# Kernel tuning notes

Measured on AMD Instinct MI355X. Metric: run time of the kernel, lower is better.

Reference implementation:

```python
import jax, jax.numpy as jnp
import numpy as np

DECAY = 0.9  # decay_const buffer (learn_decay=False)


def setup_inputs() -> dict:
    key = jax.random.key(0)
    ks = jax.random.split(key, 6)
    B, T, D = 64, 512, 768
    spk_hist = jax.random.normal(ks[0], (B, T, D), dtype=jnp.float32)
    act_hist = jax.random.normal(ks[1], (B, T, D), dtype=jnp.float32)
    spk_mask = jax.random.randint(ks[2], (B, T), 0, 2).astype(jnp.float32)
    act_mask = jax.random.randint(ks[3], (B, T), 0, 2).astype(jnp.float32)
    spk_mean = jax.random.normal(ks[4], (B, D), dtype=jnp.float32)
    act_mean = jax.random.normal(ks[5], (B, D), dtype=jnp.float32)
    mix_logits = jnp.zeros((2,), dtype=jnp.float32)
    return {"spk_hist": spk_hist, "spk_mask": spk_mask,
            "act_hist": act_hist, "act_mask": act_mask,
            "spk_mean": spk_mean, "act_mean": act_mean,
            "mix_logits": mix_logits}


def ema_pool(X, mask, decay):
    # X: [B,T,D], mask: [B,T] (1 valid, 0 pad) -> (h [B,D], has_any [B])
    B, T, D = X.shape
    one_minus = 1.0 - decay

    def step(carry, xm):
        h, has_any = carry          # [B,D], [B,1]
        xt, mt = xm                 # [B,D], [B]
        mt = mt[:, None]            # [B,1]
        h_new = decay * h + one_minus * xt
        h = mt * h_new + (1.0 - mt) * h
        has_any = jnp.minimum(has_any + mt, 1.0)
        return (h, has_any), None

    h0 = jnp.zeros((B, D), X.dtype)
    a0 = jnp.zeros((B, 1), X.dtype)
    (h, has_any), _ = jax.lax.scan(
        step, (h0, a0), (jnp.swapaxes(X, 0, 1), mask.T))
    return h, has_any[:, 0]


def reference(spk_hist, spk_mask, act_hist, act_mask, spk_mean, act_mean, mix_logits):
    c_spk, spk_nonempty = ema_pool(spk_hist, spk_mask, DECAY)
    c_act, act_nonempty = ema_pool(act_hist, act_mask, DECAY)
    c_spk = jnp.where((spk_nonempty == 0)[:, None], spk_mean, c_spk)
    c_act = jnp.where((act_nonempty == 0)[:, None], act_mean, c_act)
    w = jax.nn.softmax(mix_logits, axis=0)
    c = w[0] * c_spk + w[1] * c_act
    return (c, c_spk, c_act, w)
```

## Files before the change

kernel.cpp:

```cpp
#include <hip/hip_runtime.h>

#define B 64
#define T 512
#define D 768
#define NSEG 8
#define TSEG 64
#define LOG2_DECAY (-0.15200309344504995f)

#define WS_H  0
#define WS_NE (2 * B * D)
#define WS_W  (2 * B * D + 2 * B)

__global__ __launch_bounds__(512) void weights_kernel(
    const float* __restrict__ spk_mask, const float* __restrict__ act_mask,
    float* __restrict__ ws)
{
    const int b = blockIdx.x & (B - 1);
    const int s = blockIdx.x >> 6;
    const float* mask = s ? act_mask : spk_mask;

    const int t = threadIdx.x;
    const float m = mask[b * T + t];
    const bool on = m > 0.5f;

    const unsigned long long bal = __ballot(on);
    const int lane = t & 63;
    const int wave = t >> 6;

    __shared__ int wtot[8];
    if (lane == 0) wtot[wave] = __popcll(bal);
    __syncthreads();

    int Ct = __popcll(bal & (~0ull >> (63 - lane)));
    int S = 0;
    #pragma unroll
    for (int i = 0; i < 8; ++i) {
        int c = wtot[i];
        if (i < wave) Ct += c;
        S += c;
    }

    const float w = on ? 0.1f * exp2f((float)(S - Ct) * LOG2_DECAY) : 0.0f;
    ws[WS_W + (s * B + b) * T + t] = w;
    if (t == 0) ws[WS_NE + s * B + b] = (S > 0) ? 1.0f : 0.0f;
}

__global__ __launch_bounds__(192) void pool_kernel(
    const float* __restrict__ spk_hist, const float* __restrict__ act_hist,
    float* __restrict__ ws)
{
    const int blk = blockIdx.x;
    const int seg = blk & (NSEG - 1);
    const int b   = (blk >> 3) & (B - 1);
    const int s   = blk >> 9;

    __shared__ float wsm[TSEG];
    const int tid = threadIdx.x;
    if (tid < TSEG)
        wsm[tid] = ws[WS_W + (s * B + b) * T + seg * TSEG + tid];
    __syncthreads();

    const float* hist = s ? act_hist : spk_hist;
    const float4* X = (const float4*)(hist + (size_t)(b * T + seg * TSEG) * D) + tid;

    float4 acc = make_float4(0.f, 0.f, 0.f, 0.f);
    for (int tt = 0; tt < TSEG; ++tt) {
        const float w = wsm[tt];
        if (w != 0.0f) {
            const float4 x = X[tt * (D / 4)];
            acc.x = fmaf(w, x.x, acc.x);
            acc.y = fmaf(w, x.y, acc.y);
            acc.z = fmaf(w, x.z, acc.z);
            acc.w = fmaf(w, x.w, acc.w);
        }
    }

    float* hdst = ws + WS_H + (size_t)(s * B + b) * D + tid * 4;
    atomicAdd(hdst + 0, acc.x);
    atomicAdd(hdst + 1, acc.y);
    atomicAdd(hdst + 2, acc.z);
    atomicAdd(hdst + 3, acc.w);
}

__global__ __launch_bounds__(256) void epilogue_kernel(
    const float* __restrict__ spk_mean, const float* __restrict__ act_mean,
    const float* __restrict__ logits, const float* __restrict__ ws,
    float* __restrict__ out)
{
    const int idx = blockIdx.x * 256 + threadIdx.x;
    if (idx >= B * D) return;
    const int b = idx / D;

    const float l0 = logits[0], l1 = logits[1];
    const float mx = fmaxf(l0, l1);
    const float e0 = expf(l0 - mx), e1 = expf(l1 - mx);
    const float inv = 1.0f / (e0 + e1);
    const float w0 = e0 * inv, w1 = e1 * inv;

    const float cs = (ws[WS_NE + b]     > 0.0f) ? ws[WS_H + idx]          : spk_mean[idx];
    const float ca = (ws[WS_NE + B + b] > 0.0f) ? ws[WS_H + B * D + idx]  : act_mean[idx];

    out[idx]             = w0 * cs + w1 * ca;
    out[B * D + idx]     = cs;
    out[2 * B * D + idx] = ca;
    if (idx == 0) {
        out[3 * B * D]     = w0;
        out[3 * B * D + 1] = w1;
    }
}

extern "C" void kernel_launch(void* const* d_in, const int* in_sizes, int n_in,
                              void* d_out, int out_size, void* d_ws, size_t ws_size,
                              hipStream_t stream) {
    const float* spk_hist = (const float*)d_in[0];
    const float* spk_mask = (const float*)d_in[1];
    const float* act_hist = (const float*)d_in[2];
    const float* act_mask = (const float*)d_in[3];
    const float* spk_mean = (const float*)d_in[4];
    const float* act_mean = (const float*)d_in[5];
    const float* logits   = (const float*)d_in[6];
    float* ws  = (float*)d_ws;
    float* out = (float*)d_out;

    hipMemsetAsync(ws, 0, (size_t)(2 * B * D) * sizeof(float), stream);

    weights_kernel<<<2 * B, 512, 0, stream>>>(spk_mask, act_mask, ws);
    pool_kernel<<<2 * B * NSEG, 192, 0, stream>>>(spk_hist, act_hist, ws);
    epilogue_kernel<<<(B * D + 255) / 256, 256, 0, stream>>>(spk_mean, act_mean, logits, ws, out);
}
```

Baseline: 217.0 us.

## Fuse mask weight computation into pool kernel and replace atomics with partial sums

Drops the separate weights kernel and the memset. Each pool block recomputes the mask prefix counts and decay weights for its own segment, then compacts the valid timesteps so the load loop runs only over them, unrolled by four. Per-segment partial sums are written to the workspace without atomics and reduced in a vectorised epilogue. This removes two launches and the atomic traffic, at the cost of redundant mask scans in every block and an extra partial-sum buffer pass.

Result: faster. 207.9 us (-4.2%).

```diff
diff --git a/kernel.cpp b/kernel.cpp
--- a/kernel.cpp
+++ b/kernel.cpp
@@ -7,46 +7,12 @@
 #define TSEG 64
 #define LOG2_DECAY (-0.15200309344504995f)
 
-#define WS_H  0
-#define WS_NE (2 * B * D)
-#define WS_W  (2 * B * D + 2 * B)
-
-__global__ __launch_bounds__(512) void weights_kernel(
-    const float* __restrict__ spk_mask, const float* __restrict__ act_mask,
-    float* __restrict__ ws)
-{
-    const int b = blockIdx.x & (B - 1);
-    const int s = blockIdx.x >> 6;
-    const float* mask = s ? act_mask : spk_mask;
-
-    const int t = threadIdx.x;
-    const float m = mask[b * T + t];
-    const bool on = m > 0.5f;
-
-    const unsigned long long bal = __ballot(on);
-    const int lane = t & 63;
-    const int wave = t >> 6;
-
-    __shared__ int wtot[8];
-    if (lane == 0) wtot[wave] = __popcll(bal);
-    __syncthreads();
-
-    int Ct = __popcll(bal & (~0ull >> (63 - lane)));
-    int S = 0;
-    #pragma unroll
-    for (int i = 0; i < 8; ++i) {
-        int c = wtot[i];
-        if (i < wave) Ct += c;
-        S += c;
-    }
-
-    const float w = on ? 0.1f * exp2f((float)(S - Ct) * LOG2_DECAY) : 0.0f;
-    ws[WS_W + (s * B + b) * T + t] = w;
-    if (t == 0) ws[WS_NE + s * B + b] = (S > 0) ? 1.0f : 0.0f;
-}
+#define WS_P  0
+#define WS_NE (2 * B * NSEG * D)
 
 __global__ __launch_bounds__(192) void pool_kernel(
     const float* __restrict__ spk_hist, const float* __restrict__ act_hist,
+    const float* __restrict__ spk_mask, const float* __restrict__ act_mask,
     float* __restrict__ ws)
 {
     const int blk = blockIdx.x;
@@ -54,32 +20,93 @@
     const int b   = (blk >> 3) & (B - 1);
     const int s   = blk >> 9;
 
-    __shared__ float wsm[TSEG];
-    const int tid = threadIdx.x;
-    if (tid < TSEG)
-        wsm[tid] = ws[WS_W + (s * B + b) * T + seg * TSEG + tid];
+    const int tid  = threadIdx.x;
+    const int lane = tid & 63;
+    const int wave = tid >> 6;
+
+    __shared__ float    wsm[TSEG];
+    __shared__ float    cw[TSEG];
+    __shared__ int      ct[TSEG];
+    __shared__ unsigned wt[2];
+    __shared__ int      Mcnt;
+
+    const float* mask = s ? act_mask : spk_mask;
+    unsigned bits = 0, cnt = 0;
+    if (tid < 128) {
+        const float4 mv = ((const float4*)(mask + b * T))[tid];
+        bits = (mv.x > 0.5f ? 1u : 0u) | (mv.y > 0.5f ? 2u : 0u) |
+               (mv.z > 0.5f ? 4u : 0u) | (mv.w > 0.5f ? 8u : 0u);
+        cnt = __popc(bits);
+    }
+    unsigned v = cnt;
+    #pragma unroll
+    for (int off = 1; off < 64; off <<= 1) {
+        const unsigned u = __shfl_up(v, off);
+        if (lane >= off) v += u;
+    }
+    if (wave < 2 && lane == 63) wt[wave] = v;
+    __syncthreads();
+    const unsigned S = wt[0] + wt[1];
+
+    if (tid >= seg * 16 && tid < (seg + 1) * 16) {
+        unsigned run = (v - cnt) + (wave == 1 ? wt[0] : 0u);
+        const int lbase = (tid - seg * 16) * 4;
+        #pragma unroll
+        for (int j = 0; j < 4; ++j) {
+            float w = 0.0f;
+            if (bits & (1u << j)) {
+                run += 1;
+                w = 0.1f * exp2f((float)(S - run) * LOG2_DECAY);
+            }
+            wsm[lbase + j] = w;
+        }
+    }
+    __syncthreads();
+
+    if (tid < 64) {
+        const float wv = wsm[tid];
+        const unsigned long long bal = __ballot(wv != 0.0f);
+        if (wv != 0.0f) {
+            const int pos = __popcll(bal & ((1ull << tid) - 1ull));
+            cw[pos] = wv;
+            ct[pos] = tid;
+        }
+        if (tid == 0) Mcnt = __popcll(bal);
+    }
     __syncthreads();
 
     const float* hist = s ? act_hist : spk_hist;
-    const float4* X = (const float4*)(hist + (size_t)(b * T + seg * TSEG) * D) + tid;
+    const float* Xb = hist + (size_t)(b * T + seg * TSEG) * D + tid * 4;
 
     float4 acc = make_float4(0.f, 0.f, 0.f, 0.f);
-    for (int tt = 0; tt < TSEG; ++tt) {
-        const float w = wsm[tt];
-        if (w != 0.0f) {
-            const float4 x = X[tt * (D / 4)];
-            acc.x = fmaf(w, x.x, acc.x);
-            acc.y = fmaf(w, x.y, acc.y);
-            acc.z = fmaf(w, x.z, acc.z);
-            acc.w = fmaf(w, x.w, acc.w);
-        }
+    const int M = Mcnt;
+    int k = 0;
+    for (; k + 4 <= M; k += 4) {
+        const int   t0 = ct[k],   t1 = ct[k+1], t2 = ct[k+2], t3 = ct[k+3];
+        const float w0 = cw[k],   w1 = cw[k+1], w2 = cw[k+2], w3 = cw[k+3];
+        const float4 x0 = *(const float4*)(Xb + t0 * D);
+        const float4 x1 = *(const float4*)(Xb + t1 * D);
+        const float4 x2 = *(const float4*)(Xb + t2 * D);
+        const float4 x3 = *(const float4*)(Xb + t3 * D);
+        acc.x = fmaf(w0, x0.x, acc.x); acc.y = fmaf(w0, x0.y, acc.y);
+        acc.z = fmaf(w0, x0.z, acc.z); acc.w = fmaf(w0, x0.w, acc.w);
+        acc.x = fmaf(w1, x1.x, acc.x); acc.y = fmaf(w1, x1.y, acc.y);
+        acc.z = fmaf(w1, x1.z, acc.z); acc.w = fmaf(w1, x1.w, acc.w);
+        acc.x = fmaf(w2, x2.x, acc.x); acc.y = fmaf(w2, x2.y, acc.y);
+        acc.z = fmaf(w2, x2.z, acc.z); acc.w = fmaf(w2, x2.w, acc.w);
+        acc.x = fmaf(w3, x3.x, acc.x); acc.y = fmaf(w3, x3.y, acc.y);
+        acc.z = fmaf(w3, x3.z, acc.z); acc.w = fmaf(w3, x3.w, acc.w);
+    }
+    for (; k < M; ++k) {
+        const float w = cw[k];
+        const float4 x = *(const float4*)(Xb + ct[k] * D);
+        acc.x = fmaf(w, x.x, acc.x); acc.y = fmaf(w, x.y, acc.y);
+        acc.z = fmaf(w, x.z, acc.z); acc.w = fmaf(w, x.w, acc.w);
     }
 
-    float* hdst = ws + WS_H + (size_t)(s * B + b) * D + tid * 4;
-    atomicAdd(hdst + 0, acc.x);
-    atomicAdd(hdst + 1, acc.y);
-    atomicAdd(hdst + 2, acc.z);
-    atomicAdd(hdst + 3, acc.w);
+    *(float4*)(ws + WS_P + ((size_t)((s * B + b) * NSEG + seg)) * D + tid * 4) = acc;
+    if (tid == 0 && seg == 0)
+        ws[WS_NE + s * B + b] = (S > 0) ? 1.0f : 0.0f;
 }
 
 __global__ __launch_bounds__(256) void epilogue_kernel(
@@ -87,23 +114,43 @@
     const float* __restrict__ logits, const float* __restrict__ ws,
     float* __restrict__ out)
 {
-    const int idx = blockIdx.x * 256 + threadIdx.x;
-    if (idx >= B * D) return;
-    const int b = idx / D;
+    const int i4 = blockIdx.x * 256 + threadIdx.x;
+    if (i4 >= B * D / 4) return;
+    const int b   = i4 / (D / 4);
+    const int idx = i4 * 4;
+    const int dd  = idx - b * D;
+
+    float4 hs = make_float4(0.f, 0.f, 0.f, 0.f);
+    float4 ha = make_float4(0.f, 0.f, 0.f, 0.f);
+    #pragma unroll
+    for (int seg = 0; seg < NSEG; ++seg) {
+        const float4 ps = *(const float4*)(ws + WS_P + (size_t)((0 * B + b) * NSEG + seg) * D + dd);
+        const float4 pa = *(const float4*)(ws + WS_P + (size_t)((1 * B + b) * NSEG + seg) * D + dd);
+        hs.x += ps.x; hs.y += ps.y; hs.z += ps.z; hs.w += ps.w;
+        ha.x += pa.x; ha.y += pa.y; ha.z += pa.z; ha.w += pa.w;
+    }
 
     const float l0 = logits[0], l1 = logits[1];
     const float mx = fmaxf(l0, l1);
-    const float e0 = expf(l0 - mx), e1 = expf(l1 - mx);
+    const float e0 = __expf(l0 - mx), e1 = __expf(l1 - mx);
     const float inv = 1.0f / (e0 + e1);
     const float w0 = e0 * inv, w1 = e1 * inv;
 
-    const float cs = (ws[WS_NE + b]     > 0.0f) ? ws[WS_H + idx]          : spk_mean[idx];
-    const float ca = (ws[WS_NE + B + b] > 0.0f) ? ws[WS_H + B * D + idx]  : act_mean[idx];
+    const bool nes = ws[WS_NE + b]     > 0.0f;
+    const bool nea = ws[WS_NE + B + b] > 0.0f;
+    const float4 cs = nes ? hs : *(const float4*)(spk_mean + idx);
+    const float4 ca = nea ? ha : *(const float4*)(act_mean + idx);
 
-    out[idx]             = w0 * cs + w1 * ca;
-    out[B * D + idx]     = cs;
-    out[2 * B * D + idx] = ca;
-    if (idx == 0) {
+    float4 c;
+    c.x = w0 * cs.x + w1 * ca.x;
+    c.y = w0 * cs.y + w1 * ca.y;
+    c.z = w0 * cs.z + w1 * ca.z;
+    c.w = w0 * cs.w + w1 * ca.w;
+
+    *(float4*)(out + idx)             = c;
+    *(float4*)(out + B * D + idx)     = cs;
+    *(float4*)(out + 2 * B * D + idx) = ca;
+    if (i4 == 0) {
         out[3 * B * D]     = w0;
         out[3 * B * D + 1] = w1;
     }
@@ -122,9 +169,6 @@
     float* ws  = (float*)d_ws;
     float* out = (float*)d_out;
 
-    hipMemsetAsync(ws, 0, (size_t)(2 * B * D) * sizeof(float), stream);
-
-    weights_kernel<<<2 * B, 512, 0, stream>>>(spk_mask, act_mask, ws);
-    pool_kernel<<<2 * B * NSEG, 192, 0, stream>>>(spk_hist, act_hist, ws);
-    epilogue_kernel<<<(B * D + 255) / 256, 256, 0, stream>>>(spk_mean, act_mean, logits, ws, out);
+    pool_kernel<<<2 * B * NSEG, 192, 0, stream>>>(spk_hist, act_hist, spk_mask, act_mask, ws);
+    epilogue_kernel<<<(B * D / 4 + 255) / 256, 256, 0, stream>>>(spk_mean, act_mean, logits, ws, out);
 }
```
